# Kernel tuning notes

Measured on AMD Instinct MI355X. Metric: run time of the kernel, lower is better.

Reference implementation:

```python
import jax, jax.numpy as jnp
import numpy as np


def _smooth_l1(x, y):
    # PyTorch F.smooth_l1_loss elementwise with beta=1.0
    d = jnp.abs(x - y)
    return jnp.where(d < 1.0, 0.5 * d * d, d - 0.5)


def setup_inputs() -> dict:
    key = jax.random.key(0)
    k1, k2, k3 = jax.random.split(key, 3)
    B, S, N, D = 2, 8, 2048, 3
    X_v = jax.random.normal(k1, (B, S, N, D), dtype=jnp.float32)
    target_X_v = jax.random.normal(k2, (B, S, N, D), dtype=jnp.float32)
    weights = jax.random.uniform(k3, (B, S), dtype=jnp.float32)
    return {"X_v": X_v, "target_X_v": target_X_v, "weights": weights}


def reference(X_v, target_X_v, weights):
    B, S, N, D = X_v.shape
    # Pairwise squared distances via ||p||^2 + ||t||^2 - 2 p.t  -> [B,S,N,N]
    p2 = jnp.sum(X_v * X_v, axis=-1)            # [B,S,N]
    t2 = jnp.sum(target_X_v * target_X_v, axis=-1)
    cross = jnp.einsum('bsnd,bsmd->bsnm', X_v, target_X_v)
    dist = p2[..., :, None] + t2[..., None, :] - 2.0 * cross
    # Chamfer nearest-neighbor indices (argmin is non-differentiable, as in torch)
    minv = jnp.argmin(dist, axis=-1)   # for each pred point: nearest target [B,S,N]
    minvy = jnp.argmin(dist, axis=-2)  # for each target point: nearest pred
    tagp = jnp.take_along_axis(target_X_v, minv[..., None], axis=2)   # [B,S,N,3]
    predd = jnp.take_along_axis(X_v, minvy[..., None], axis=2)
    tmp1 = jnp.mean(_smooth_l1(X_v, tagp), axis=(-1, -2))       # [B,S]
    tmp2 = jnp.mean(_smooth_l1(target_X_v, predd), axis=(-1, -2))
    per_set = tmp1 + tmp2
    loss = jnp.sum(per_set * weights) / B
    # Centroid loss
    prec = jnp.mean(X_v, axis=2)        # [B,S,3]
    tarc = jnp.mean(target_X_v, axis=2)
    lossc = jnp.sum(_smooth_l1(prec, tarc)) / (B * 3)
    return (loss, lossc)
```

## Files before the change

### kernel.cpp

```cpp
#include <hip/hip_runtime.h>
#include <math.h>

#define N_PTS 2048
#define N_SETS 16
#define B_VAL 2.0f
#define BLOCK 256

__device__ __forceinline__ float sl1(float d) {
    d = fabsf(d);
    return d < 1.0f ? 0.5f * d * d : d - 0.5f;
}

__global__ void init_out_kernel(float* out) {
    out[0] = 0.0f;
    out[1] = 0.0f;
}

__global__ __launch_bounds__(BLOCK) void chamfer_kernel(
    const float* __restrict__ X, const float* __restrict__ T,
    const float* __restrict__ W, float* __restrict__ out)
{
    const int chunk = blockIdx.x;
    const int set   = blockIdx.y;
    const int dir   = blockIdx.z;

    const float* qsrc = (dir == 0) ? (T + (size_t)set * N_PTS * 3)
                                   : (X + (size_t)set * N_PTS * 3);
    const float* psrc = (dir == 0) ? (X + (size_t)set * N_PTS * 3)
                                   : (T + (size_t)set * N_PTS * 3);

    __shared__ float qx[N_PTS];
    __shared__ float qy[N_PTS];
    __shared__ float qz[N_PTS];
    __shared__ float q2[N_PTS];
    __shared__ float wpart[4];

    const int tid = threadIdx.x;

    for (int j = tid; j < N_PTS * 3; j += BLOCK) {
        float v = qsrc[j];
        int pt = j / 3;
        int d  = j - pt * 3;
        if (d == 0) qx[pt] = v;
        else if (d == 1) qy[pt] = v;
        else qz[pt] = v;
    }
    __syncthreads();
    for (int i = tid; i < N_PTS; i += BLOCK) {
        float a = qx[i], b = qy[i], c = qz[i];
        q2[i] = a * a + b * b + c * c;
    }
    __syncthreads();

    const int n = chunk * BLOCK + tid;
    const float px = psrc[n * 3 + 0];
    const float py = psrc[n * 3 + 1];
    const float pz = psrc[n * 3 + 2];
    const float px2 = -2.0f * px;
    const float py2 = -2.0f * py;
    const float pz2 = -2.0f * pz;

    float b0 = INFINITY, b1 = INFINITY, b2 = INFINITY, b3 = INFINITY;
    int   i0 = 0, i1 = 0, i2 = 0, i3 = 0;

    const float4* qx4 = reinterpret_cast<const float4*>(qx);
    const float4* qy4 = reinterpret_cast<const float4*>(qy);
    const float4* qz4 = reinterpret_cast<const float4*>(qz);
    const float4* q24 = reinterpret_cast<const float4*>(q2);

#pragma unroll 4
    for (int m4 = 0; m4 < N_PTS / 4; ++m4) {
        float4 vx = qx4[m4];
        float4 vy = qy4[m4];
        float4 vz = qz4[m4];
        float4 vh = q24[m4];
        float d0 = fmaf(px2, vx.x, fmaf(py2, vy.x, fmaf(pz2, vz.x, vh.x)));
        float d1 = fmaf(px2, vx.y, fmaf(py2, vy.y, fmaf(pz2, vz.y, vh.y)));
        float d2 = fmaf(px2, vx.z, fmaf(py2, vy.z, fmaf(pz2, vz.z, vh.z)));
        float d3 = fmaf(px2, vx.w, fmaf(py2, vy.w, fmaf(pz2, vz.w, vh.w)));
        if (d0 < b0) { b0 = d0; i0 = m4; }
        if (d1 < b1) { b1 = d1; i1 = m4; }
        if (d2 < b2) { b2 = d2; i2 = m4; }
        if (d3 < b3) { b3 = d3; i3 = m4; }
    }

    float bb = b0; int bi = i0 * 4 + 0;
    {
        int g1 = i1 * 4 + 1;
        if (b1 < bb || (b1 == bb && g1 < bi)) { bb = b1; bi = g1; }
        int g2 = i2 * 4 + 2;
        if (b2 < bb || (b2 == bb && g2 < bi)) { bb = b2; bi = g2; }
        int g3 = i3 * 4 + 3;
        if (b3 < bb || (b3 == bb && g3 < bi)) { bb = b3; bi = g3; }
    }

    float s = sl1(px - qx[bi]) + sl1(py - qy[bi]) + sl1(pz - qz[bi]);

    for (int off = 32; off > 0; off >>= 1)
        s += __shfl_down(s, off, 64);
    if ((tid & 63) == 0) wpart[tid >> 6] = s;
    __syncthreads();
    if (tid == 0) {
        float tot = wpart[0] + wpart[1] + wpart[2] + wpart[3];
        atomicAdd(&out[0], W[set] * tot * (1.0f / (N_PTS * 3.0f * B_VAL)));
    }
}

__global__ __launch_bounds__(BLOCK) void centroid_kernel(
    const float* __restrict__ X, const float* __restrict__ T,
    float* __restrict__ out)
{
    const int set = blockIdx.x;
    const int tid = threadIdx.x;
    const float* xb = X + (size_t)set * N_PTS * 3;
    const float* tb = T + (size_t)set * N_PTS * 3;

    float acc[6] = {0, 0, 0, 0, 0, 0};
    for (int i = tid; i < N_PTS; i += BLOCK) {
        acc[0] += xb[i * 3 + 0];
        acc[1] += xb[i * 3 + 1];
        acc[2] += xb[i * 3 + 2];
        acc[3] += tb[i * 3 + 0];
        acc[4] += tb[i * 3 + 1];
        acc[5] += tb[i * 3 + 2];
    }

    __shared__ float red[6][BLOCK];
    for (int k = 0; k < 6; ++k) red[k][tid] = acc[k];
    __syncthreads();
    for (int sft = BLOCK / 2; sft > 0; sft >>= 1) {
        if (tid < sft)
            for (int k = 0; k < 6; ++k) red[k][tid] += red[k][tid + sft];
        __syncthreads();
    }
    if (tid == 0) {
        const float inv = 1.0f / (float)N_PTS;
        float l = sl1(red[0][0] * inv - red[3][0] * inv)
                + sl1(red[1][0] * inv - red[4][0] * inv)
                + sl1(red[2][0] * inv - red[5][0] * inv);
        atomicAdd(&out[1], l * (1.0f / (B_VAL * 3.0f)));
    }
}

extern "C" void kernel_launch(void* const* d_in, const int* in_sizes, int n_in,
                              void* d_out, int out_size, void* d_ws, size_t ws_size,
                              hipStream_t stream) {
    const float* X = (const float*)d_in[0];
    const float* T = (const float*)d_in[1];
    const float* W = (const float*)d_in[2];
    float* out = (float*)d_out;

    init_out_kernel<<<1, 1, 0, stream>>>(out);
    centroid_kernel<<<N_SETS, BLOCK, 0, stream>>>(X, T, out);
    chamfer_kernel<<<dim3(N_PTS / BLOCK, N_SETS, 2), BLOCK, 0, stream>>>(X, T, W, out);
}
```

Baseline: 97.81 us.

## Split chamfer search over candidate segments with 64-bit atomicMin argmin merge

Restructures the nearest-neighbour search. Each block now takes a 128-candidate segment of one set and direction, and each thread handles 8 query points, reusing every candidate loaded from shared memory across those 8 queries. Per-segment minima are packed as an order-preserving float key plus index into 64-bit values and merged with atomicMin into a workspace, and a separate finalize kernel then gathers the chosen neighbours and computes the smooth-L1 sum. The output zeroing moves into the first block, the centroid reduction switches to wave shuffles, and a memset and extra kernel launch are added; if the centroid kernel's atomic runs before that zeroing, the result could race.

```diff
diff --git a/kernel.cpp b/kernel.cpp
--- a/kernel.cpp
+++ b/kernel.cpp
@@ -5,97 +5,106 @@
 #define N_SETS 16
 #define B_VAL 2.0f
 #define BLOCK 256
+#define SEGS 16
+#define CPS (N_PTS / SEGS)
+#define QPT 8
 
 __device__ __forceinline__ float sl1(float d) {
     d = fabsf(d);
     return d < 1.0f ? 0.5f * d * d : d - 0.5f;
 }
 
-__global__ void init_out_kernel(float* out) {
-    out[0] = 0.0f;
-    out[1] = 0.0f;
+__device__ __forceinline__ unsigned int fkey(float f) {
+    unsigned int b = __float_as_uint(f);
+    return (b & 0x80000000u) ? ~b : (b | 0x80000000u);
 }
 
-__global__ __launch_bounds__(BLOCK) void chamfer_kernel(
+__global__ __launch_bounds__(BLOCK) void chamfer_partial(
     const float* __restrict__ X, const float* __restrict__ T,
-    const float* __restrict__ W, float* __restrict__ out)
+    unsigned long long* __restrict__ ws, float* __restrict__ out)
+{
+    const int seg = blockIdx.x;
+    const int set = blockIdx.y;
+    const int dir = blockIdx.z;
+    const int tid = threadIdx.x;
+
+    if (seg == 0 && set == 0 && dir == 0 && tid == 0) {
+        out[0] = 0.0f;
+        out[1] = 0.0f;
+    }
+
+    const float* psrc = (dir == 0) ? (X + (size_t)set * N_PTS * 3)
+                                   : (T + (size_t)set * N_PTS * 3);
+    const float* csrc = (dir == 0) ? (T + (size_t)set * N_PTS * 3)
+                                   : (X + (size_t)set * N_PTS * 3);
+
+    __shared__ float4 cand[CPS];
+    if (tid < CPS) {
+        const int g = seg * CPS + tid;
+        float cx = csrc[g * 3 + 0];
+        float cy = csrc[g * 3 + 1];
+        float cz = csrc[g * 3 + 2];
+        cand[tid] = make_float4(cx, cy, cz, cx * cx + cy * cy + cz * cz);
+    }
+    __syncthreads();
+
+    float ax[QPT], ay[QPT], az[QPT];
+    float best[QPT];
+    int   bidx[QPT];
+#pragma unroll
+    for (int j = 0; j < QPT; ++j) {
+        const int q = tid + BLOCK * j;
+        ax[j] = -2.0f * psrc[q * 3 + 0];
+        ay[j] = -2.0f * psrc[q * 3 + 1];
+        az[j] = -2.0f * psrc[q * 3 + 2];
+        best[j] = INFINITY;
+        bidx[j] = 0;
+    }
+
+#pragma unroll 4
+    for (int m = 0; m < CPS; ++m) {
+        float4 c = cand[m];
+#pragma unroll
+        for (int j = 0; j < QPT; ++j) {
+            float d = fmaf(ax[j], c.x, fmaf(ay[j], c.y, fmaf(az[j], c.z, c.w)));
+            if (d < best[j]) { best[j] = d; bidx[j] = m; }
+        }
+    }
+
+    unsigned long long* wq = ws + ((size_t)(set * 2 + dir) << 11);
+#pragma unroll
+    for (int j = 0; j < QPT; ++j) {
+        const int q = tid + BLOCK * j;
+        const unsigned int gidx = (unsigned int)(seg * CPS + bidx[j]);
+        unsigned long long key = ((unsigned long long)fkey(best[j]) << 32) | gidx;
+        atomicMin(&wq[q], key);
+    }
+}
+
+__global__ __launch_bounds__(BLOCK) void finalize_kernel(
+    const float* __restrict__ X, const float* __restrict__ T,
+    const float* __restrict__ W, const unsigned long long* __restrict__ ws,
+    float* __restrict__ out)
 {
     const int chunk = blockIdx.x;
     const int set   = blockIdx.y;
     const int dir   = blockIdx.z;
+    const int tid   = threadIdx.x;
+    const int n     = chunk * BLOCK + tid;
 
-    const float* qsrc = (dir == 0) ? (T + (size_t)set * N_PTS * 3)
-                                   : (X + (size_t)set * N_PTS * 3);
     const float* psrc = (dir == 0) ? (X + (size_t)set * N_PTS * 3)
                                    : (T + (size_t)set * N_PTS * 3);
+    const float* csrc = (dir == 0) ? (T + (size_t)set * N_PTS * 3)
+                                   : (X + (size_t)set * N_PTS * 3);
 
-    __shared__ float qx[N_PTS];
-    __shared__ float qy[N_PTS];
-    __shared__ float qz[N_PTS];
-    __shared__ float q2[N_PTS];
+    const unsigned long long key = ws[((size_t)(set * 2 + dir) << 11) + n];
+    const unsigned int idx = (unsigned int)(key & 0xFFFFFFFFu);
+
+    float s = sl1(psrc[n * 3 + 0] - csrc[idx * 3 + 0])
+            + sl1(psrc[n * 3 + 1] - csrc[idx * 3 + 1])
+            + sl1(psrc[n * 3 + 2] - csrc[idx * 3 + 2]);
+
     __shared__ float wpart[4];
-
-    const int tid = threadIdx.x;
-
-    for (int j = tid; j < N_PTS * 3; j += BLOCK) {
-        float v = qsrc[j];
-        int pt = j / 3;
-        int d  = j - pt * 3;
-        if (d == 0) qx[pt] = v;
-        else if (d == 1) qy[pt] = v;
-        else qz[pt] = v;
-    }
-    __syncthreads();
-    for (int i = tid; i < N_PTS; i += BLOCK) {
-        float a = qx[i], b = qy[i], c = qz[i];
-        q2[i] = a * a + b * b + c * c;
-    }
-    __syncthreads();
-
-    const int n = chunk * BLOCK + tid;
-    const float px = psrc[n * 3 + 0];
-    const float py = psrc[n * 3 + 1];
-    const float pz = psrc[n * 3 + 2];
-    const float px2 = -2.0f * px;
-    const float py2 = -2.0f * py;
-    const float pz2 = -2.0f * pz;
-
-    float b0 = INFINITY, b1 = INFINITY, b2 = INFINITY, b3 = INFINITY;
-    int   i0 = 0, i1 = 0, i2 = 0, i3 = 0;
-
-    const float4* qx4 = reinterpret_cast<const float4*>(qx);
-    const float4* qy4 = reinterpret_cast<const float4*>(qy);
-    const float4* qz4 = reinterpret_cast<const float4*>(qz);
-    const float4* q24 = reinterpret_cast<const float4*>(q2);
-
-#pragma unroll 4
-    for (int m4 = 0; m4 < N_PTS / 4; ++m4) {
-        float4 vx = qx4[m4];
-        float4 vy = qy4[m4];
-        float4 vz = qz4[m4];
-        float4 vh = q24[m4];
-        float d0 = fmaf(px2, vx.x, fmaf(py2, vy.x, fmaf(pz2, vz.x, vh.x)));
-        float d1 = fmaf(px2, vx.y, fmaf(py2, vy.y, fmaf(pz2, vz.y, vh.y)));
-        float d2 = fmaf(px2, vx.z, fmaf(py2, vy.z, fmaf(pz2, vz.z, vh.z)));
-        float d3 = fmaf(px2, vx.w, fmaf(py2, vy.w, fmaf(pz2, vz.w, vh.w)));
-        if (d0 < b0) { b0 = d0; i0 = m4; }
-        if (d1 < b1) { b1 = d1; i1 = m4; }
-        if (d2 < b2) { b2 = d2; i2 = m4; }
-        if (d3 < b3) { b3 = d3; i3 = m4; }
-    }
-
-    float bb = b0; int bi = i0 * 4 + 0;
-    {
-        int g1 = i1 * 4 + 1;
-        if (b1 < bb || (b1 == bb && g1 < bi)) { bb = b1; bi = g1; }
-        int g2 = i2 * 4 + 2;
-        if (b2 < bb || (b2 == bb && g2 < bi)) { bb = b2; bi = g2; }
-        int g3 = i3 * 4 + 3;
-        if (b3 < bb || (b3 == bb && g3 < bi)) { bb = b3; bi = g3; }
-    }
-
-    float s = sl1(px - qx[bi]) + sl1(py - qy[bi]) + sl1(pz - qz[bi]);
-
     for (int off = 32; off > 0; off >>= 1)
         s += __shfl_down(s, off, 64);
     if ((tid & 63) == 0) wpart[tid >> 6] = s;
@@ -125,19 +134,25 @@
         acc[5] += tb[i * 3 + 2];
     }
 
-    __shared__ float red[6][BLOCK];
-    for (int k = 0; k < 6; ++k) red[k][tid] = acc[k];
+#pragma unroll
+    for (int k = 0; k < 6; ++k)
+        for (int off = 32; off > 0; off >>= 1)
+            acc[k] += __shfl_down(acc[k], off, 64);
+
+    __shared__ float red[4][6];
+    if ((tid & 63) == 0)
+#pragma unroll
+        for (int k = 0; k < 6; ++k) red[tid >> 6][k] = acc[k];
     __syncthreads();
-    for (int sft = BLOCK / 2; sft > 0; sft >>= 1) {
-        if (tid < sft)
-            for (int k = 0; k < 6; ++k) red[k][tid] += red[k][tid + sft];
-        __syncthreads();
-    }
     if (tid == 0) {
         const float inv = 1.0f / (float)N_PTS;
-        float l = sl1(red[0][0] * inv - red[3][0] * inv)
-                + sl1(red[1][0] * inv - red[4][0] * inv)
-                + sl1(red[2][0] * inv - red[5][0] * inv);
+        float l = 0.0f;
+#pragma unroll
+        for (int k = 0; k < 3; ++k) {
+            float a = (red[0][k] + red[1][k] + red[2][k] + red[3][k]) * inv;
+            float b = (red[0][k + 3] + red[1][k + 3] + red[2][k + 3] + red[3][k + 3]) * inv;
+            l += sl1(a - b);
+        }
         atomicAdd(&out[1], l * (1.0f / (B_VAL * 3.0f)));
     }
 }
@@ -149,8 +164,11 @@
     const float* T = (const float*)d_in[1];
     const float* W = (const float*)d_in[2];
     float* out = (float*)d_out;
+    unsigned long long* ws = (unsigned long long*)d_ws;
 
-    init_out_kernel<<<1, 1, 0, stream>>>(out);
+    hipMemsetAsync(d_ws, 0xFF, (size_t)N_SETS * 2 * N_PTS * sizeof(unsigned long long), stream);
+
+    chamfer_partial<<<dim3(SEGS, N_SETS, 2), BLOCK, 0, stream>>>(X, T, ws, out);
     centroid_kernel<<<N_SETS, BLOCK, 0, stream>>>(X, T, out);
-    chamfer_kernel<<<dim3(N_PTS / BLOCK, N_SETS, 2), BLOCK, 0, stream>>>(X, T, W, out);
+    finalize_kernel<<<dim3(N_PTS / BLOCK, N_SETS, 2), BLOCK, 0, stream>>>(X, T, W, ws, out);
 }
```

Measured after the change: 89.04 us. 1.1x faster.
